# Performance work log

Measured on AMD Instinct MI355X. Metric: run time of the kernel, lower is better.

The kernel has to match this reference:

```python
import jax, jax.numpy as jnp
import numpy as np

N_NODES = 50000
N_EDGES = 800000
IN_DIM = 128
HID_DIM = 128
NUM_GRAPHS = 64


def gcn_conv(x, edge_index, W, b):
    """PyG GCNConv: symmetric-normalized aggregation with self-loops.
    out = D^{-1/2} (A + I) D^{-1/2} (x @ W) + b
    """
    n = x.shape[0]
    loop = jnp.arange(n, dtype=edge_index.dtype)
    src = jnp.concatenate([edge_index[0], loop])  # [E+N]
    dst = jnp.concatenate([edge_index[1], loop])
    deg = jax.ops.segment_sum(jnp.ones_like(dst, x.dtype), dst, num_segments=n)
    dinv = jnp.where(deg > 0, jax.lax.rsqrt(deg), 0.0)
    norm = dinv[src] * dinv[dst]  # [E+N]
    h = x @ W  # [N, H] transform before propagate (PyG order)
    msg = h[src] * norm[:, None]  # [E+N, H] gathered+scaled messages
    out = jax.ops.segment_sum(msg, dst, num_segments=n)  # scatter-add
    return out + b


def global_mean_pool(x, batch, num_graphs):
    s = jax.ops.segment_sum(x, batch, num_segments=num_graphs)
    cnt = jax.ops.segment_sum(jnp.ones((x.shape[0],), x.dtype), batch, num_segments=num_graphs)
    return s / jnp.maximum(cnt, 1.0)[:, None]


def setup_inputs() -> dict:
    key = jax.random.key(0)
    ks = jax.random.split(key, 8)
    x = jax.random.normal(ks[0], (N_NODES, IN_DIM), dtype=jnp.float32)
    edge_index = jax.random.randint(ks[1], (2, N_EDGES), 0, N_NODES, dtype=jnp.int64)
    batch = jnp.sort(jax.random.randint(ks[2], (N_NODES,), 0, NUM_GRAPHS, dtype=jnp.int64))
    s1 = 1.0 / np.sqrt(IN_DIM)
    s2 = 1.0 / np.sqrt(HID_DIM)
    W1 = jax.random.uniform(ks[3], (IN_DIM, HID_DIM), jnp.float32, -s1, s1)
    b1 = jnp.zeros((HID_DIM,), jnp.float32)
    W2 = jax.random.uniform(ks[4], (HID_DIM, HID_DIM), jnp.float32, -s2, s2)
    b2 = jnp.zeros((HID_DIM,), jnp.float32)
    Wc = jax.random.uniform(ks[5], (HID_DIM, 1), jnp.float32, -s2, s2)
    bc = jnp.zeros((1,), jnp.float32)
    return {"x": x, "edge_index": edge_index, "batch": batch,
            "W1": W1, "b1": b1, "W2": W2, "b2": b2, "Wc": Wc, "bc": bc}


def reference(x, edge_index, batch, W1, b1, W2, b2, Wc, bc):
    h = jax.nn.relu(gcn_conv(x, edge_index, W1, b1))
    # dropout p=0.1 is identity in eval mode
    h = gcn_conv(h, edge_index, W2, b2)
    g = global_mean_pool(h, batch, NUM_GRAPHS)  # [G, H]
    return jax.nn.sigmoid(g @ Wc + bc)  # [G, 1]
```

## Files before the change

### kernel.cpp

```cpp
#include <hip/hip_runtime.h>
#include <hip/hip_bf16.h>
#include <hip/hip_fp16.h>

#define N_NODES 50000
#define N_EDGES 800000
#define DIM     128
#define NG      64
#define GN      16
#define CAP     48
#define NSUB    8
#define CAPSUB  12
#define AGG_EB  256
#define LAXP    136

#define FILL_B  391
#define CAST_B  1563
#define VB_B    129
#define WF_B    8

typedef float  f2_t  __attribute__((ext_vector_type(2)));
typedef float  f32x4 __attribute__((ext_vector_type(4)));
typedef _Float16 f16x8 __attribute__((ext_vector_type(8)));
typedef _Float16 f16x4 __attribute__((ext_vector_type(4)));

__global__ void k_prep(const int* __restrict__ ei, int* __restrict__ cur,
                       unsigned short* __restrict__ csrS,
                       const float4* __restrict__ x4, uint4* __restrict__ xq4,
                       const float* __restrict__ W2, const float* __restrict__ Wc,
                       const float* __restrict__ b2, float* __restrict__ v,
                       float* __restrict__ beta2,
                       const float* __restrict__ W1, f16x8* __restrict__ w1f) {
    __shared__ float red[4];
    int bid = blockIdx.x, t = threadIdx.x;
    if (bid < FILL_B) {
        int sub = bid & (NSUB - 1);
        int* mycur = cur + sub * N_NODES;
        int base = bid * 2048 + t;
        int ss[8], dd[8]; bool vv[8];
        #pragma unroll
        for (int k = 0; k < 8; k++) {
            int e = base + k * 256;
            vv[k] = (e < N_EDGES);
            int ec = vv[k] ? e : 0;
            ss[k] = ei[ec]; dd[k] = ei[N_EDGES + ec];
        }
        int pos[8];
        #pragma unroll
        for (int k = 0; k < 8; k++)
            pos[k] = vv[k] ? atomicAdd(&mycur[dd[k]], 1) : CAPSUB;
        #pragma unroll
        for (int k = 0; k < 8; k++)
            if (pos[k] < CAPSUB)
                csrS[((size_t)dd[k] * NSUB + sub) * CAPSUB + pos[k]] = (unsigned short)ss[k];
    } else if (bid < FILL_B + CAST_B) {
        int idx = (bid - FILL_B) * 256 + t;
        if (idx < N_NODES * DIM / 16) {
            uint4 o;
            unsigned* op = (unsigned*)&o;
            #pragma unroll
            for (int q = 0; q < 4; q++) {
                float4 f = x4[idx * 4 + q];
                int p = 0;
                p = __builtin_amdgcn_cvt_pk_fp8_f32(f.x, f.y, p, false);
                p = __builtin_amdgcn_cvt_pk_fp8_f32(f.z, f.w, p, true);
                op[q] = (unsigned)p;
            }
            xq4[idx] = o;
        }
    } else if (bid < FILL_B + CAST_B + VB_B) {
        int b = bid - (FILL_B + CAST_B);
        float p = 0.f;
        if (t < DIM) p = (b < DIM) ? W2[b * DIM + t] * Wc[t] : b2[t] * Wc[t];
        #pragma unroll
        for (int off = 32; off > 0; off >>= 1) p += __shfl_down(p, off, 64);
        if ((t & 63) == 0) red[t >> 6] = p;
        __syncthreads();
        if (t == 0) {
            float s = red[0] + red[1];
            if (b < DIM) v[b] = s; else beta2[0] = s;
        }
    } else {
        int idx = (bid - (FILL_B + CAST_B + VB_B)) * 256 + t;
        int ntile = idx >> 8, kb = (idx >> 6) & 3, l = idx & 63;
        int kbase = kb * 32 + (l >> 4) * 8;
        int n = ntile * 16 + (l & 15);
        f16x8 o;
        #pragma unroll
        for (int j = 0; j < 8; j++) o[j] = (_Float16)W1[(kbase + j) * DIM + n];
        w1f[idx] = o;
    }
}

__global__ void k_dinv(const int* __restrict__ cur, float* __restrict__ dinv) {
    int i = blockIdx.x * 256 + threadIdx.x;
    if (i < N_NODES) {
        int d = 0;
        #pragma unroll
        for (int s = 0; s < NSUB; s++) d += cur[s * N_NODES + i];
        dinv[i] = rsqrtf((float)(d + 1));
    }
}

__global__ void k_compact(const int* __restrict__ cur, const float* __restrict__ dinv,
                          const unsigned short* __restrict__ csrS,
                          unsigned int* __restrict__ csr, int* __restrict__ degS) {
    int tid = blockIdx.x * 256 + threadIdx.x;
    if (tid >= N_NODES * NSUB) return;
    int n = tid >> 3, sub = tid & (NSUB - 1);
    int pref = 0, mycnt = 0, tot = 0;
    #pragma unroll
    for (int s = 0; s < NSUB; s++) {
        int c = min(cur[s * N_NODES + n], CAPSUB);
        if (s < sub) pref += c;
        if (s == sub) mycnt = c;
        tot += c;
    }
    if (sub == 0) degS[n] = min(tot, CAP);
    for (int j = 0; j < mycnt; j++) {
        int pos = pref + j;
        if (pos >= CAP) break;
        unsigned ssrc = csrS[((size_t)n * NSUB + sub) * CAPSUB + j];
        unsigned hw = (unsigned)__half_as_ushort(__float2half(dinv[ssrc]));
        csr[(size_t)n * CAP + pos] = ssrc | (hw << 16);
    }
}

__global__ __launch_bounds__(512) void k_node(
    const unsigned int* __restrict__ xq,
    const unsigned int* __restrict__ csr,
    const f16x8* __restrict__ w1f,
    const float* __restrict__ b1,
    const float* __restrict__ v, const float* __restrict__ dinv,
    const int* __restrict__ degS, float* __restrict__ z2) {
    __shared__ _Float16 laxh[GN * LAXP];
    __shared__ float redm[GN * 8];
    int tid = threadIdx.x;
    int w = tid >> 6, l = tid & 63;
    int half = l >> 5, hl = l & 31;
    int node0 = blockIdx.x * GN;

    {
        int i = node0 + 2 * w + half;
        int start = i * CAP;
        int len = degS[i];
        int lm1 = (len > 0) ? len - 1 : 0;
        float di = dinv[i];

        unsigned su = xq[(size_t)i * 32 + hl];
        f2_t s01 = __builtin_amdgcn_cvt_pk_f32_fp8((int)su, false);
        f2_t s23 = __builtin_amdgcn_cvt_pk_f32_fp8((int)su, true);
        float a0 = di * s01.x, a1 = di * s01.y;
        float a2 = di * s23.x, a3 = di * s23.y;
        float b0 = 0.f, b1_ = 0.f, b2_ = 0.f, b3 = 0.f;
        float c0 = 0.f, c1 = 0.f, c2 = 0.f, c3 = 0.f;
        float d0 = 0.f, d1 = 0.f, d2 = 0.f, d3 = 0.f;

        int lenmax = max(len, __shfl_xor(len, 32, 64));
        for (int j = 0; j < lenmax; j += 4) {
            int j0 = min(j + 0, lm1), j1 = min(j + 1, lm1);
            int j2 = min(j + 2, lm1), j3 = min(j + 3, lm1);
            unsigned p0 = csr[start + j0];
            unsigned p1 = csr[start + j1];
            unsigned p2 = csr[start + j2];
            unsigned p3 = csr[start + j3];
            float w0 = (j + 0 < len) ? __half2float(__ushort_as_half((unsigned short)(p0 >> 16))) : 0.f;
            float w1 = (j + 1 < len) ? __half2float(__ushort_as_half((unsigned short)(p1 >> 16))) : 0.f;
            float w2 = (j + 2 < len) ? __half2float(__ushort_as_half((unsigned short)(p2 >> 16))) : 0.f;
            float w3 = (j + 3 < len) ? __half2float(__ushort_as_half((unsigned short)(p3 >> 16))) : 0.f;
            unsigned q0 = xq[(size_t)(p0 & 0xFFFFu) * 32 + hl];
            unsigned q1 = xq[(size_t)(p1 & 0xFFFFu) * 32 + hl];
            unsigned q2 = xq[(size_t)(p2 & 0xFFFFu) * 32 + hl];
            unsigned q3 = xq[(size_t)(p3 & 0xFFFFu) * 32 + hl];
            f2_t e01, e23;
            e01 = __builtin_amdgcn_cvt_pk_f32_fp8((int)q0, false);
            e23 = __builtin_amdgcn_cvt_pk_f32_fp8((int)q0, true);
            a0 = fmaf(w0, e01.x, a0); a1 = fmaf(w0, e01.y, a1);
            a2 = fmaf(w0, e23.x, a2); a3 = fmaf(w0, e23.y, a3);
            e01 = __builtin_amdgcn_cvt_pk_f32_fp8((int)q1, false);
            e23 = __builtin_amdgcn_cvt_pk_f32_fp8((int)q1, true);
            b0 = fmaf(w1, e01.x, b0); b1_ = fmaf(w1, e01.y, b1_);
            b2_ = fmaf(w1, e23.x, b2_); b3 = fmaf(w1, e23.y, b3);
            e01 = __builtin_amdgcn_cvt_pk_f32_fp8((int)q2, false);
            e23 = __builtin_amdgcn_cvt_pk_f32_fp8((int)q2, true);
            c0 = fmaf(w2, e01.x, c0); c1 = fmaf(w2, e01.y, c1);
            c2 = fmaf(w2, e23.x, c2); c3 = fmaf(w2, e23.y, c3);
            e01 = __builtin_amdgcn_cvt_pk_f32_fp8((int)q3, false);
            e23 = __builtin_amdgcn_cvt_pk_f32_fp8((int)q3, true);
            d0 = fmaf(w3, e01.x, d0); d1 = fmaf(w3, e01.y, d1);
            d2 = fmaf(w3, e23.x, d2); d3 = fmaf(w3, e23.y, d3);
        }
        a0 += b0 + c0 + d0; a1 += b1_ + c1 + d1;
        a2 += b2_ + c2 + d2; a3 += b3 + c3 + d3;
        f16x4 pk;
        pk[0] = (_Float16)(di * a0); pk[1] = (_Float16)(di * a1);
        pk[2] = (_Float16)(di * a2); pk[3] = (_Float16)(di * a3);
        *(f16x4*)&laxh[(2 * w + half) * LAXP + 4 * hl] = pk;
    }
    __syncthreads();

    f32x4 acc = {0.f, 0.f, 0.f, 0.f};
    #pragma unroll
    for (int kb = 0; kb < 4; kb++) {
        f16x8 af = *(const f16x8*)&laxh[(l & 15) * LAXP + kb * 32 + (l >> 4) * 8];
        f16x8 bf = w1f[(w * 4 + kb) * 64 + l];
        acc = __builtin_amdgcn_mfma_f32_16x16x32_f16(af, bf, acc, 0, 0, 0);
    }
    int n = w * 16 + (l & 15);
    float bn = b1[n], vn = v[n];
    #pragma unroll
    for (int r = 0; r < 4; r++) {
        float p = fmaxf(acc[r] + bn, 0.f) * vn;
        p += __shfl_xor(p, 1, 64);
        p += __shfl_xor(p, 2, 64);
        p += __shfl_xor(p, 4, 64);
        p += __shfl_xor(p, 8, 64);
        if ((l & 15) == 0) redm[((l >> 4) * 4 + r) * 8 + w] = p;
    }
    __syncthreads();
    if (tid < GN) {
        float s = 0.f;
        #pragma unroll
        for (int q = 0; q < 8; q++) s += redm[tid * 8 + q];
        z2[node0 + tid] = dinv[node0 + tid] * s;
    }
}

__global__ void k_aggz(const float* __restrict__ z2, const float* __restrict__ dinv,
                       const int* __restrict__ ei, const int* __restrict__ batch,
                       float* __restrict__ gpartE, float* __restrict__ gpartN,
                       int* __restrict__ gcnt) {
    int bid = blockIdx.x, t = threadIdx.x;
    if (bid < AGG_EB) {
        __shared__ float bs[4][NG];
        bs[t >> 6][t & 63] = 0.f;
        __syncthreads();
        int wg = t >> 6;
        for (int base = bid * 1024; base < N_EDGES; base += AGG_EB * 1024) {
            #pragma unroll
            for (int k = 0; k < 4; k++) {
                int e = base + k * 256 + t;
                if (e < N_EDGES) {
                    int s = ei[e];
                    int d = ei[N_EDGES + e];
                    atomicAdd(&bs[wg][batch[d]], dinv[d] * z2[s]);
                }
            }
        }
        __syncthreads();
        if (t < NG) gpartE[bid * NG + t] = bs[0][t] + bs[1][t] + bs[2][t] + bs[3][t];
    } else {
        __shared__ int range[2];
        __shared__ float rs[4];
        int g = bid - AGG_EB;
        if (t < 2) {
            int key = g + t;
            int lo = 0, hi = N_NODES;
            while (lo < hi) { int m = (lo + hi) >> 1; if (batch[m] < key) lo = m + 1; else hi = m; }
            range[t] = lo;
        }
        __syncthreads();
        int lo = range[0], hi = range[1];
        float loc = 0.f;
        for (int i = lo + t; i < hi; i += 256) loc += dinv[i] * z2[i];
        #pragma unroll
        for (int off = 32; off > 0; off >>= 1) loc += __shfl_down(loc, off, 64);
        if ((t & 63) == 0) rs[t >> 6] = loc;
        __syncthreads();
        if (t == 0) {
            gpartN[g] = rs[0] + rs[1] + rs[2] + rs[3];
            gcnt[g] = hi - lo;
        }
    }
}

__global__ void k_final(const float* __restrict__ gpartE, const float* __restrict__ gpartN,
                        const int* __restrict__ gcnt, const float* __restrict__ beta2,
                        const float* __restrict__ bcin, float* __restrict__ out) {
    __shared__ float acc[4][NG];
    int t = threadIdx.x;
    int g = t & 63, c = t >> 6;
    float s = 0.f;
    for (int k = 0; k < AGG_EB / 4; k++)
        s += gpartE[(c * (AGG_EB / 4) + k) * NG + g];
    acc[c][g] = s;
    __syncthreads();
    if (t < NG) {
        float tot = acc[0][t] + acc[1][t] + acc[2][t] + acc[3][t] + gpartN[t];
        int cnt = gcnt[t];
        float val = tot / (float)(cnt > 0 ? cnt : 1) + beta2[0] + bcin[0];
        out[t] = 1.f / (1.f + expf(-val));
    }
}

extern "C" void kernel_launch(void* const* d_in, const int* in_sizes, int n_in,
                              void* d_out, int out_size, void* d_ws, size_t ws_size,
                              hipStream_t stream) {
    const float* x   = (const float*)d_in[0];
    const int*   ei  = (const int*)  d_in[1];
    const int*   bat = (const int*)  d_in[2];
    const float* W1  = (const float*)d_in[3];
    const float* b1  = (const float*)d_in[4];
    const float* W2  = (const float*)d_in[5];
    const float* b2  = (const float*)d_in[6];
    const float* Wc  = (const float*)d_in[7];
    const float* bc  = (const float*)d_in[8];
    float* out = (float*)d_out;

    char* w = (char*)d_ws;
    size_t off = 0;
    auto alloc = [&](size_t bytes) -> void* {
        void* p = w + off;
        off = (off + bytes + 255) & ~(size_t)255;
        return p;
    };
    int*   cur     = (int*)  alloc((size_t)NSUB * N_NODES * 4);
    size_t zero_len = off;
    float* dinv    = (float*)alloc(N_NODES * 4);
    int*   degS    = (int*)  alloc(N_NODES * 4);
    float* z2      = (float*)alloc(N_NODES * 4);
    float* v       = (float*)alloc(DIM * 4);
    float* beta2   = (float*)alloc(4);
    float* gpartE  = (float*)alloc((size_t)AGG_EB * NG * 4);
    float* gpartN  = (float*)alloc(NG * 4);
    int*   gcnt    = (int*)  alloc(NG * 4);
    f16x8* w1f     = (f16x8*)alloc(2048 * 16);
    unsigned int*   xq   = (unsigned int*)  alloc((size_t)N_NODES * DIM);
    unsigned short* csrS = (unsigned short*)alloc((size_t)N_NODES * NSUB * CAPSUB * 2);
    unsigned int*   csr  = (unsigned int*)  alloc((size_t)N_NODES * CAP * 4);
    (void)ws_size; (void)in_sizes; (void)n_in; (void)out_size;

    hipMemsetAsync(d_ws, 0, zero_len, stream);

    dim3 b256(256);
    k_prep<<<dim3(FILL_B + CAST_B + VB_B + WF_B), b256, 0, stream>>>(
        ei, cur, csrS, (const float4*)x, (uint4*)xq, W2, Wc, b2, v, beta2, W1, w1f);
    k_dinv<<<dim3((N_NODES + 255) / 256), b256, 0, stream>>>(cur, dinv);
    k_compact<<<dim3((N_NODES * NSUB + 255) / 256), b256, 0, stream>>>(cur, dinv, csrS, csr, degS);
    k_node<<<dim3(N_NODES / GN), dim3(512), 0, stream>>>(
        xq, csr, w1f, b1, v, dinv, degS, z2);
    k_aggz<<<dim3(AGG_EB + NG), b256, 0, stream>>>(z2, dinv, ei, bat, gpartE, gpartN, gcnt);
    k_final<<<dim3(1), b256, 0, stream>>>(gpartE, gpartN, gcnt, beta2, bc, out);
}
```

Baseline: 184.8 us.

## Build CSR directly with single counter array and drop dinv/compact kernels

Replaces the sub-partitioned CSR fill (8 counter copies plus a compaction pass) with a direct atomic fill into the final fixed-capacity CSR, one edge per thread. A new stamp kernel then packs the fp16 source degree-normalization into each CSR entry, and the separate dinv array is removed in favor of recomputing rsqrt from the counts wherever it is needed. This removes two kernels and the intermediate buffer, but concentrates atomics on one counter array and scatters CSR writes. The stamp kernel also launches over all capacity slots rather than only filled ones.

Measured after the change: 183.4 us. No clear change (-0.8%).

```diff
diff --git a/kernel.cpp b/kernel.cpp
--- a/kernel.cpp
+++ b/kernel.cpp
@@ -8,12 +8,10 @@
 #define NG      64
 #define GN      16
 #define CAP     48
-#define NSUB    8
-#define CAPSUB  12
 #define AGG_EB  256
 #define LAXP    136
 
-#define FILL_B  391
+#define FILL_B  3125
 #define CAST_B  1563
 #define VB_B    129
 #define WF_B    8
@@ -24,7 +22,7 @@
 typedef _Float16 f16x4 __attribute__((ext_vector_type(4)));
 
 __global__ void k_prep(const int* __restrict__ ei, int* __restrict__ cur,
-                       unsigned short* __restrict__ csrS,
+                       unsigned int* __restrict__ csr,
                        const float4* __restrict__ x4, uint4* __restrict__ xq4,
                        const float* __restrict__ W2, const float* __restrict__ Wc,
                        const float* __restrict__ b2, float* __restrict__ v,
@@ -33,25 +31,11 @@
     __shared__ float red[4];
     int bid = blockIdx.x, t = threadIdx.x;
     if (bid < FILL_B) {
-        int sub = bid & (NSUB - 1);
-        int* mycur = cur + sub * N_NODES;
-        int base = bid * 2048 + t;
-        int ss[8], dd[8]; bool vv[8];
-        #pragma unroll
-        for (int k = 0; k < 8; k++) {
-            int e = base + k * 256;
-            vv[k] = (e < N_EDGES);
-            int ec = vv[k] ? e : 0;
-            ss[k] = ei[ec]; dd[k] = ei[N_EDGES + ec];
-        }
-        int pos[8];
-        #pragma unroll
-        for (int k = 0; k < 8; k++)
-            pos[k] = vv[k] ? atomicAdd(&mycur[dd[k]], 1) : CAPSUB;
-        #pragma unroll
-        for (int k = 0; k < 8; k++)
-            if (pos[k] < CAPSUB)
-                csrS[((size_t)dd[k] * NSUB + sub) * CAPSUB + pos[k]] = (unsigned short)ss[k];
+        int e = bid * 256 + t;
+        int s = ei[e];
+        int d = ei[N_EDGES + e];
+        int pos = atomicAdd(&cur[d], 1);
+        if (pos < CAP) csr[d * CAP + pos] = (unsigned)s;
     } else if (bid < FILL_B + CAST_B) {
         int idx = (bid - FILL_B) * 256 + t;
         if (idx < N_NODES * DIM / 16) {
@@ -91,37 +75,17 @@
     }
 }
 
-__global__ void k_dinv(const int* __restrict__ cur, float* __restrict__ dinv) {
-    int i = blockIdx.x * 256 + threadIdx.x;
-    if (i < N_NODES) {
-        int d = 0;
-        #pragma unroll
-        for (int s = 0; s < NSUB; s++) d += cur[s * N_NODES + i];
-        dinv[i] = rsqrtf((float)(d + 1));
-    }
-}
-
-__global__ void k_compact(const int* __restrict__ cur, const float* __restrict__ dinv,
-                          const unsigned short* __restrict__ csrS,
-                          unsigned int* __restrict__ csr, int* __restrict__ degS) {
-    int tid = blockIdx.x * 256 + threadIdx.x;
-    if (tid >= N_NODES * NSUB) return;
-    int n = tid >> 3, sub = tid & (NSUB - 1);
-    int pref = 0, mycnt = 0, tot = 0;
-    #pragma unroll
-    for (int s = 0; s < NSUB; s++) {
-        int c = min(cur[s * N_NODES + n], CAPSUB);
-        if (s < sub) pref += c;
-        if (s == sub) mycnt = c;
-        tot += c;
-    }
-    if (sub == 0) degS[n] = min(tot, CAP);
-    for (int j = 0; j < mycnt; j++) {
-        int pos = pref + j;
-        if (pos >= CAP) break;
-        unsigned ssrc = csrS[((size_t)n * NSUB + sub) * CAPSUB + j];
-        unsigned hw = (unsigned)__half_as_ushort(__float2half(dinv[ssrc]));
-        csr[(size_t)n * CAP + pos] = ssrc | (hw << 16);
+__global__ void k_stamp(const int* __restrict__ cur, unsigned int* __restrict__ csr) {
+    int idx = blockIdx.x * 256 + threadIdx.x;
+    if (idx >= N_NODES * CAP) return;
+    int n = idx / CAP;
+    int slot = idx - n * CAP;
+    int deg = min(cur[n], CAP);
+    if (slot < deg) {
+        unsigned e = csr[idx] & 0xFFFFu;
+        float w = rsqrtf((float)cur[e] + 1.f);
+        unsigned hw = (unsigned)__half_as_ushort(__float2half(w));
+        csr[idx] = e | (hw << 16);
     }
 }
 
@@ -130,8 +94,8 @@
     const unsigned int* __restrict__ csr,
     const f16x8* __restrict__ w1f,
     const float* __restrict__ b1,
-    const float* __restrict__ v, const float* __restrict__ dinv,
-    const int* __restrict__ degS, float* __restrict__ z2) {
+    const float* __restrict__ v, const int* __restrict__ cur,
+    float* __restrict__ z2) {
     __shared__ _Float16 laxh[GN * LAXP];
     __shared__ float redm[GN * 8];
     int tid = threadIdx.x;
@@ -142,9 +106,9 @@
     {
         int i = node0 + 2 * w + half;
         int start = i * CAP;
-        int len = degS[i];
+        int len = min(cur[i], CAP);
         int lm1 = (len > 0) ? len - 1 : 0;
-        float di = dinv[i];
+        float di = rsqrtf((float)cur[i] + 1.f);
 
         unsigned su = xq[(size_t)i * 32 + hl];
         f2_t s01 = __builtin_amdgcn_cvt_pk_f32_fp8((int)su, false);
@@ -221,11 +185,11 @@
         float s = 0.f;
         #pragma unroll
         for (int q = 0; q < 8; q++) s += redm[tid * 8 + q];
-        z2[node0 + tid] = dinv[node0 + tid] * s;
-    }
-}
-
-__global__ void k_aggz(const float* __restrict__ z2, const float* __restrict__ dinv,
+        z2[node0 + tid] = rsqrtf((float)cur[node0 + tid] + 1.f) * s;
+    }
+}
+
+__global__ void k_aggz(const float* __restrict__ z2, const int* __restrict__ cur,
                        const int* __restrict__ ei, const int* __restrict__ batch,
                        float* __restrict__ gpartE, float* __restrict__ gpartN,
                        int* __restrict__ gcnt) {
@@ -242,7 +206,8 @@
                 if (e < N_EDGES) {
                     int s = ei[e];
                     int d = ei[N_EDGES + e];
-                    atomicAdd(&bs[wg][batch[d]], dinv[d] * z2[s]);
+                    float dv = rsqrtf((float)cur[d] + 1.f);
+                    atomicAdd(&bs[wg][batch[d]], dv * z2[s]);
                 }
             }
         }
@@ -261,7 +226,8 @@
         __syncthreads();
         int lo = range[0], hi = range[1];
         float loc = 0.f;
-        for (int i = lo + t; i < hi; i += 256) loc += dinv[i] * z2[i];
+        for (int i = lo + t; i < hi; i += 256)
+            loc += rsqrtf((float)cur[i] + 1.f) * z2[i];
         #pragma unroll
         for (int off = 32; off > 0; off >>= 1) loc += __shfl_down(loc, off, 64);
         if ((t & 63) == 0) rs[t >> 6] = loc;
@@ -313,10 +279,8 @@
         off = (off + bytes + 255) & ~(size_t)255;
         return p;
     };
-    int*   cur     = (int*)  alloc((size_t)NSUB * N_NODES * 4);
+    int*   cur     = (int*)  alloc(N_NODES * 4);
     size_t zero_len = off;
-    float* dinv    = (float*)alloc(N_NODES * 4);
-    int*   degS    = (int*)  alloc(N_NODES * 4);
     float* z2      = (float*)alloc(N_NODES * 4);
     float* v       = (float*)alloc(DIM * 4);
     float* beta2   = (float*)alloc(4);
@@ -324,20 +288,18 @@
     float* gpartN  = (float*)alloc(NG * 4);
     int*   gcnt    = (int*)  alloc(NG * 4);
     f16x8* w1f     = (f16x8*)alloc(2048 * 16);
-    unsigned int*   xq   = (unsigned int*)  alloc((size_t)N_NODES * DIM);
-    unsigned short* csrS = (unsigned short*)alloc((size_t)N_NODES * NSUB * CAPSUB * 2);
-    unsigned int*   csr  = (unsigned int*)  alloc((size_t)N_NODES * CAP * 4);
+    unsigned int* xq  = (unsigned int*)alloc((size_t)N_NODES * DIM);
+    unsigned int* csr = (unsigned int*)alloc((size_t)N_NODES * CAP * 4);
     (void)ws_size; (void)in_sizes; (void)n_in; (void)out_size;
 
     hipMemsetAsync(d_ws, 0, zero_len, stream);
 
     dim3 b256(256);
     k_prep<<<dim3(FILL_B + CAST_B + VB_B + WF_B), b256, 0, stream>>>(
-        ei, cur, csrS, (const float4*)x, (uint4*)xq, W2, Wc, b2, v, beta2, W1, w1f);
-    k_dinv<<<dim3((N_NODES + 255) / 256), b256, 0, stream>>>(cur, dinv);
-    k_compact<<<dim3((N_NODES * NSUB + 255) / 256), b256, 0, stream>>>(cur, dinv, csrS, csr, degS);
+        ei, cur, csr, (const float4*)x, (uint4*)xq, W2, Wc, b2, v, beta2, W1, w1f);
+    k_stamp<<<dim3((N_NODES * CAP + 255) / 256), b256, 0, stream>>>(cur, csr);
     k_node<<<dim3(N_NODES / GN), dim3(512), 0, stream>>>(
-        xq, csr, w1f, b1, v, dinv, degS, z2);
-    k_aggz<<<dim3(AGG_EB + NG), b256, 0, stream>>>(z2, dinv, ei, bat, gpartE, gpartN, gcnt);
+        xq, csr, w1f, b1, v, cur, z2);
+    k_aggz<<<dim3(AGG_EB + NG), b256, 0, stream>>>(z2, cur, ei, bat, gpartE, gpartN, gcnt);
     k_final<<<dim3(1), b256, 0, stream>>>(gpartE, gpartN, gcnt, beta2, bc, out);
 }
```
